# Optimization experiments

Measured on AMD Instinct MI355X. Metric: run time of the kernel, lower is better.

The kernel has to match this reference:

```python
import jax, jax.numpy as jnp
import numpy as np
from jax import lax

N_SAMPLES = 2 ** 15          # 32768
N_FRAMES = 128
N_HARMONICS = 8
FILT_SIZE = 64
N_EVENTS = 8
N_SCALE = 128                # len(MusicalScale()) assumed = 128 (MIDI notes)
NYQ = 11025.0                # SR22050 nyquist
MIN_F0 = 40.0 / NYQ
MAX_F0 = 3000.0 / NYQ
F0_SPAN = MAX_F0 - MIN_F0
MIN_RES = 0.9
RES_SPAN = 1.0 - MIN_RES
PI = float(np.pi)

# packed layout slices (order of param_sizes dict)
SL_F0 = slice(0, 128)
SL_FINE = slice(128, 256)
SL_AMP = slice(256, 384)
SL_HAMP = slice(384, 392)
SL_HDEC = slice(392, 400)
SL_FENV = slice(400, 464)


def lin_interp(x, out_size):
    """F.interpolate(mode='linear', align_corners=False) along last axis."""
    n = x.shape[-1]
    pos = (jnp.arange(out_size, dtype=x.dtype) + 0.5) * (n / out_size) - 0.5
    pos = jnp.clip(pos, 0.0, n - 1)
    lo = jnp.floor(pos).astype(jnp.int32)
    hi = jnp.minimum(lo + 1, n - 1)
    w = pos - lo.astype(x.dtype)
    return x[..., lo] * (1.0 - w) + x[..., hi] * w


def setup_inputs() -> dict:
    key = jax.random.key(0)
    k1, k2 = jax.random.split(key)
    B = 32 * N_EVENTS  # 256 event rows
    packed = jax.random.normal(k1, (B, 464), dtype=jnp.float32)
    # musical scale: MIDI-note center frequencies normalized by nyquist
    midi = np.arange(N_SCALE)
    freqs = 440.0 * 2.0 ** ((midi - 69) / 12.0) / NYQ
    frequencies = jnp.asarray(freqs, dtype=jnp.float32)
    noise = jax.random.uniform(k2, (B, 1, N_SAMPLES), dtype=jnp.float32)  # mapped to (-1,1) in reference
    return {"packed": packed, "frequencies": frequencies, "noise": noise}


def reference(packed, frequencies, noise):
    B = packed.shape[0]
    p = jax.nn.sigmoid(packed)  # Model applies activation(p) before SynthParams

    # f0: softmax over discrete scale bins, weighted sum of normalized freqs
    f0w = jax.nn.softmax(p[:, SL_F0], axis=-1)             # [B, 128]
    f0 = (f0w @ frequencies)[:, None, None]                # [B,1,1]
    f0 = jnp.broadcast_to(f0, (B, 1, N_FRAMES))            # repeat over frames
    f0 = f0 * NYQ
    f0 = MIN_F0 + f0 * F0_SPAN                             # [B,1,128]
    # NOTE: source computes `f0 + f0 + f0_fine` and discards it -> f0_fine unused

    harmonic_factors = jnp.arange(1, N_HARMONICS + 1, dtype=p.dtype)
    osc = f0 * harmonic_factors[None, :, None]             # [B,8,128]
    radians = osc / NYQ * PI
    radians = lin_interp(radians, N_SAMPLES)               # [B,8,32768]
    osc_bank = jnp.sin(jnp.cumsum(radians, axis=-1))

    harm_decay = MIN_RES + p[:, SL_HDEC] * RES_SPAN        # [B,8]
    harm_amp = p[:, SL_HAMP]                               # [B,8]
    amp = p[:, SL_AMP][:, None, :] * 2.0 - 1.0             # [B,1,128]
    amp_full = lin_interp(amp, N_SAMPLES)                  # [B,1,32768]

    noise_filter = p[:, SL_FENV][:, None, :]               # [B,1,64]
    noise_filter = lin_interp(noise_filter, N_SAMPLES // 2)
    noise_filter = jnp.pad(noise_filter, ((0, 0), (0, 0), (0, 1)))  # [B,1,16385]

    noise_u = noise * 2.0 - 1.0                            # uniform(-1,1)
    noise_spec = jnp.fft.rfft(noise_u, axis=-1, norm='ortho')
    filt = jnp.fft.irfft(noise_spec * noise_filter, n=N_SAMPLES, axis=-1, norm='ortho')
    filt = filt * jnp.clip(amp_full, 0.0, 1.0)             # [B,1,32768]

    # leaky-accumulator recurrence over frames
    def step(cur, a_i):  # cur [B,8], a_i [B]
        cur = jnp.clip(cur + a_i[:, None] * harm_amp, 0.0, 1.0)
        out = cur
        cur = cur * harm_decay
        return cur, out

    amp_t = amp[:, 0, :].T                                 # [128, B]
    _, outs = lax.scan(step, jnp.zeros((B, N_HARMONICS), dtype=p.dtype), amp_t)
    x = jnp.transpose(outs, (1, 2, 0))                     # [B,8,128]
    x = jnp.where(x >= PI, 0.0, x)
    x = lin_interp(x, N_SAMPLES)                           # [B,8,32768]
    x = x * osc_bank
    x = filt + x
    x = x.reshape(-1, N_EVENTS, N_HARMONICS, N_SAMPLES)
    x = jnp.sum(x, axis=(1, 2))[:, None, :]                # [batch,1,32768]
    return x
```

## Files before the change

### kernel.cpp

```cpp
#include <hip/hip_runtime.h>
#include <math.h>

#ifndef M_PI
#define M_PI 3.14159265358979323846
#endif

#define NSAMP 32768
#define MHALF 16384
#define TWO_PI_F 6.2831853071795864f

__device__ __forceinline__ double dsig(double x) { return 1.0 / (1.0 + exp(-x)); }

__global__ __launch_bounds__(128) void prep_kernel(
    const float* __restrict__ packed, const float* __restrict__ freqs,
    unsigned long long* __restrict__ step, float* __restrict__ env,
    float* __restrict__ amp, float* __restrict__ fenv)
{
    int b = blockIdx.x;
    int t = threadIdx.x;
    const float* pk = packed + b * 464;
    __shared__ double sh_num[128];
    __shared__ double sh_den[128];
    __shared__ double amp_d[128];

    double e_t = exp(dsig((double)pk[t]));
    sh_den[t] = e_t;
    sh_num[t] = e_t * (double)freqs[t];

    double av = dsig((double)pk[256 + t]) * 2.0 - 1.0;
    amp_d[t] = av;
    amp[b * 128 + t] = (float)av;

    if (t < 64) fenv[b * 64 + t] = (float)dsig((double)pk[400 + t]);
    __syncthreads();

    for (int off = 64; off > 0; off >>= 1) {
        if (t < off) { sh_den[t] += sh_den[t + off]; sh_num[t] += sh_num[t + off]; }
        __syncthreads();
    }

    if (t < 8) {
        const double NYQ = 11025.0;
        const double MIN_F0 = 40.0 / NYQ;
        const double MAX_F0 = 3000.0 / NYQ;
        const double F0_SPAN = MAX_F0 - MIN_F0;
        double f0 = sh_num[0] / sh_den[0];
        double F = f0 * NYQ;
        double G = MIN_F0 + F * F0_SPAN;
        double oscf = G * (double)(t + 1);
        double r = oscf / NYQ * M_PI;
        double rv = r / (2.0 * M_PI);
        rv -= floor(rv);
        step[b * 8 + t] = (unsigned long long)(rv * 18446744073709551616.0);

        double ha = dsig((double)pk[384 + t]);
        double hd = 0.9 + dsig((double)pk[392 + t]) * (1.0 - 0.9);
        double cur = 0.0;
        float* eo = env + (size_t)(b * 8 + t) * 128;
        for (int fr = 0; fr < 128; fr++) {
            cur = cur + amp_d[fr] * ha;
            cur = fmin(fmax(cur, 0.0), 1.0);
            eo[fr] = (float)cur;
            cur *= hd;
        }
    }
}

__device__ __forceinline__ float2 cmulc(float2 a, float2 b) {
    return make_float2(a.x * b.x - a.y * b.y, a.x * b.y + a.y * b.x);
}
__device__ __forceinline__ float2 twid(float2 a, float ang) {
    float sn, cs; __sincosf(ang, &sn, &cs);
    return make_float2(a.x * cs - a.y * sn, a.x * sn + a.y * cs);
}

template<int INV>
__device__ __forceinline__ void fft4(float2& x0, float2& x1, float2& x2, float2& x3) {
    float2 s02 = make_float2(x0.x + x2.x, x0.y + x2.y);
    float2 d02 = make_float2(x0.x - x2.x, x0.y - x2.y);
    float2 s13 = make_float2(x1.x + x3.x, x1.y + x3.y);
    float2 d13 = make_float2(x1.x - x3.x, x1.y - x3.y);
    float2 j13 = INV ? make_float2(-d13.y, d13.x) : make_float2(d13.y, -d13.x);
    x0 = make_float2(s02.x + s13.x, s02.y + s13.y);
    x2 = make_float2(s02.x - s13.x, s02.y - s13.y);
    x1 = make_float2(d02.x + j13.x, d02.y + j13.y);
    x3 = make_float2(d02.x - j13.x, d02.y - j13.y);
}

#define V16(v, c) v[((((c) & 3) << 2) | ((c) >> 2))]

template<int INV>
__device__ __forceinline__ void fft16(float2 v[16]) {
    const float s = INV ? 1.0f : -1.0f;
#pragma unroll
    for (int b = 0; b < 4; b++) fft4<INV>(v[b], v[4 + b], v[8 + b], v[12 + b]);
    v[5]  = cmulc(v[5],  make_float2(0.9238795325f,  s * 0.3826834324f));
    v[9]  = cmulc(v[9],  make_float2(0.7071067812f,  s * 0.7071067812f));
    v[13] = cmulc(v[13], make_float2(0.3826834324f,  s * 0.9238795325f));
    v[6]  = cmulc(v[6],  make_float2(0.7071067812f,  s * 0.7071067812f));
    v[10] = cmulc(v[10], make_float2(0.0f,           s * 1.0f));
    v[14] = cmulc(v[14], make_float2(-0.7071067812f, s * 0.7071067812f));
    v[7]  = cmulc(v[7],  make_float2(0.3826834324f,  s * 0.9238795325f));
    v[11] = cmulc(v[11], make_float2(-0.7071067812f, s * 0.7071067812f));
    v[15] = cmulc(v[15], make_float2(-0.9238795325f, s * -0.3826834324f));
#pragma unroll
    for (int p = 0; p < 4; p++) fft4<INV>(v[4 * p], v[4 * p + 1], v[4 * p + 2], v[4 * p + 3]);
}

__device__ __forceinline__ int physA(int A) { return A + (A >> 6); }

__device__ __forceinline__ float hinterp64(const float* f, int j) {
    float pos = ((float)j + 0.5f) * (1.0f / 256.0f) - 0.5f;
    pos = fminf(fmaxf(pos, 0.0f), 63.0f);
    int lo = (int)pos;
    int hi = min(lo + 1, 63);
    float w = pos - (float)lo;
    return f[lo] * (1.0f - w) + f[hi] * w;
}

template<int INV>
__device__ __forceinline__ void passes234(float2* z, int tid) {
    const float sgn = INV ? 1.0f : -1.0f;
    const int c0 = tid >> 8;
    {
        const int bp = tid & 255;
        float2 v[16];
        const int base = c0 * 4096 + bp;
#pragma unroll
        for (int a = 0; a < 16; a++) v[a] = z[base + 256 * a];
        __syncthreads();
        fft16<INV>(v);
        const float w0 = sgn * (TWO_PI_F / 4096.f) * (float)bp;
        z[(c0 * 16 + 0) * 257 + bp] = V16(v, 0);
#pragma unroll
        for (int c1 = 1; c1 < 16; c1++)
            z[(c0 * 16 + c1) * 257 + bp] = twid(V16(v, c1), w0 * (float)c1);
        __syncthreads();
    }
    {
        const int c1 = (tid >> 4) & 15, b2 = tid & 15;
        float2 v[16];
        const int base = (c0 * 16 + c1) * 257 + b2;
#pragma unroll
        for (int a = 0; a < 16; a++) v[a] = z[base + 16 * a];
        __syncthreads();
        fft16<INV>(v);
        const float w0 = sgn * (TWO_PI_F / 256.f) * (float)b2;
        z[((c0 * 16 + c1) * 16 + 0) * 17 + b2] = V16(v, 0);
#pragma unroll
        for (int c2 = 1; c2 < 16; c2++)
            z[((c0 * 16 + c1) * 16 + c2) * 17 + b2] = twid(V16(v, c2), w0 * (float)c2);
        __syncthreads();
    }
    {
        const int c1 = (tid >> 4) & 15, c2 = tid & 15;
        float2 v[16];
        const int base = ((c0 * 16 + c1) * 16 + c2) * 17;
#pragma unroll
        for (int b = 0; b < 16; b++) v[b] = z[base + b];
        __syncthreads();
        fft16<INV>(v);
        const int A0 = 64 * c2 + 4 * c1 + c0;
#pragma unroll
        for (int c3 = 0; c3 < 16; c3++) {
            int A = 1024 * c3 + A0;
            z[physA(A)] = V16(v, c3);
        }
        __syncthreads();
    }
}

__global__ __launch_bounds__(1024) void fft_kernel(
    const float* __restrict__ noise, const float* __restrict__ amp,
    const float* __restrict__ fenv, float* __restrict__ filt)
{
    __shared__ float2 z[17408];
    __shared__ float fenv_s[64];
    __shared__ float amp_s[128];
    const int bb = blockIdx.x;
    const int tid = threadIdx.x;

    if (tid < 64) fenv_s[tid] = fenv[bb * 64 + tid];
    if (tid < 128) amp_s[tid] = amp[bb * 128 + tid];

    const float2* nz = (const float2*)(noise + (size_t)bb * NSAMP);

    {
        float2 v[16];
#pragma unroll
        for (int m = 0; m < 4; m++)
#pragma unroll
            for (int a = 0; a < 4; a++) {
                float2 t = nz[a * 4096 + m * 1024 + tid];
                v[m * 4 + a] = make_float2(t.x * 2.f - 1.f, t.y * 2.f - 1.f);
            }
#pragma unroll
        for (int m = 0; m < 4; m++) {
            fft4<0>(v[m * 4 + 0], v[m * 4 + 1], v[m * 4 + 2], v[m * 4 + 3]);
            float w0 = -(TWO_PI_F / 16384.f) * (float)(m * 1024 + tid);
#pragma unroll
            for (int c0 = 1; c0 < 4; c0++) v[m * 4 + c0] = twid(v[m * 4 + c0], w0 * (float)c0);
#pragma unroll
            for (int c0 = 0; c0 < 4; c0++) z[c0 * 4096 + m * 1024 + tid] = v[m * 4 + c0];
        }
    }
    __syncthreads();
    passes234<0>(z, tid);

    const float invM = 1.0f / (float)MHALF;
    for (int k = tid; k <= 8192; k += 1024) {
        if (k == 0) {
            float2 Z0 = z[physA(0)];
            float Y0 = (Z0.x + Z0.y) * hinterp64(fenv_s, 0);
            float vv = Y0 * 0.5f * invM;
            z[physA(0)] = make_float2(vv, vv);
        } else if (k == 8192) {
            float s = hinterp64(fenv_s, 8192) * invM;
            float2 Zk = z[physA(8192)];
            z[physA(8192)] = make_float2(Zk.x * s, Zk.y * s);
        } else {
            int ik = physA(k), imk = physA(16384 - k);
            float2 Zk = z[ik], Zm = z[imk];
            float Ex = 0.5f * (Zk.x + Zm.x);
            float Ey = 0.5f * (Zk.y - Zm.y);
            float Ox = 0.5f * (Zk.y + Zm.y);
            float Oy = -0.5f * (Zk.x - Zm.x);
            float ang = (float)M_PI * (float)k * (1.0f / 16384.0f);
            float sn, cs;
            __sincosf(ang, &sn, &cs);
            float Xkx = Ex + cs * Ox + sn * Oy;
            float Xky = Ey + cs * Oy - sn * Ox;
            float Xmx = Ex - cs * Ox - sn * Oy;
            float Xmy = -Ey + cs * Oy - sn * Ox;
            float Hk = hinterp64(fenv_s, k);
            float Hm = hinterp64(fenv_s, 16384 - k);
            float Ykx = Xkx * Hk, Yky = Xky * Hk;
            float Ymx = Xmx * Hm, Ymy = Xmy * Hm;
            float Er = 0.5f * (Ykx + Ymx);
            float Ei = 0.5f * (Yky - Ymy);
            float Pr = 0.5f * (Ykx - Ymx);
            float Pi = 0.5f * (Yky + Ymy);
            float Oyx = Pr * cs - Pi * sn;
            float Oyy = Pr * sn + Pi * cs;
            z[ik]  = make_float2((Er - Oyy) * invM, (Ei + Oyx) * invM);
            z[imk] = make_float2((Er + Oyy) * invM, (-Ei + Oyx) * invM);
        }
    }
    __syncthreads();

    {
        float2 v[16];
#pragma unroll
        for (int m = 0; m < 4; m++)
#pragma unroll
            for (int a = 0; a < 4; a++) {
                int A = a * 4096 + m * 1024 + tid;
                v[m * 4 + a] = z[physA(A)];
            }
        __syncthreads();
#pragma unroll
        for (int m = 0; m < 4; m++) {
            fft4<1>(v[m * 4 + 0], v[m * 4 + 1], v[m * 4 + 2], v[m * 4 + 3]);
            float w0 = (TWO_PI_F / 16384.f) * (float)(m * 1024 + tid);
#pragma unroll
            for (int c0 = 1; c0 < 4; c0++) v[m * 4 + c0] = twid(v[m * 4 + c0], w0 * (float)c0);
#pragma unroll
            for (int c0 = 0; c0 < 4; c0++) z[c0 * 4096 + m * 1024 + tid] = v[m * 4 + c0];
        }
    }
    __syncthreads();
    passes234<1>(z, tid);

    float2* fo = (float2*)(filt + (size_t)bb * NSAMP);
    for (int m = tid; m < MHALF; m += 1024) {
        float2 y = z[physA(m)];
        int s0 = 2 * m;
        float p0 = ((float)s0 + 0.5f) * (1.0f / 256.0f) - 0.5f;
        float p1 = p0 + (1.0f / 256.0f);
        p0 = fminf(fmaxf(p0, 0.0f), 127.0f);
        p1 = fminf(fmaxf(p1, 0.0f), 127.0f);
        int l0 = (int)p0, l1 = (int)p1;
        int h0 = min(l0 + 1, 127), h1 = min(l1 + 1, 127);
        float w0 = p0 - (float)l0, w1 = p1 - (float)l1;
        float a0 = amp_s[l0] * (1.0f - w0) + amp_s[h0] * w0;
        float a1 = amp_s[l1] * (1.0f - w1) + amp_s[h1] * w1;
        a0 = fminf(fmaxf(a0, 0.0f), 1.0f);
        a1 = fminf(fmaxf(a1, 0.0f), 1.0f);
        fo[m] = make_float2(y.x * a0, y.y * a1);
    }
}

__global__ __launch_bounds__(256) void synth_kernel(
    const unsigned long long* __restrict__ step, const float* __restrict__ env,
    const float* __restrict__ filt, float* __restrict__ out)
{
    const int chunk = blockIdx.x;
    const int g = blockIdx.y;
    const int tid = threadIdx.x;
    __shared__ float env_s[64 * 128];
    __shared__ unsigned long long step_s[64];

    const float* eg = env + (size_t)g * 64 * 128;
    for (int i = tid; i < 64 * 128; i += 256) env_s[i] = eg[i];
    if (tid < 64) step_s[tid] = step[g * 64 + tid];
    __syncthreads();

    const int s0 = chunk * 1024 + tid * 4;

    float4 aF = make_float4(0.f, 0.f, 0.f, 0.f);
#pragma unroll
    for (int e = 0; e < 8; e++) {
        const float4 f = *(const float4*)(filt + ((size_t)(g * 8 + e)) * NSAMP + s0);
        aF.x += f.x; aF.y += f.y; aF.z += f.z; aF.w += f.w;
    }

    float c0v[4], c1v[4], c2v[4];
    int lo0;
    {
        float pos0 = ((float)s0 + 0.5f) * (1.0f / 256.0f) - 0.5f;
        pos0 = fminf(fmaxf(pos0, 0.0f), 127.0f);
        lo0 = (int)pos0;
        int lo3 = lo0;
#pragma unroll
        for (int k = 0; k < 4; k++) {
            float pos = ((float)(s0 + k) + 0.5f) * (1.0f / 256.0f) - 0.5f;
            pos = fminf(fmaxf(pos, 0.0f), 127.0f);
            int lo = (int)pos;
            float w = pos - (float)lo;
            if (lo == lo0) { c0v[k] = 1.0f - w; c1v[k] = w;        c2v[k] = 0.0f; }
            else           { c0v[k] = 0.0f;     c1v[k] = 1.0f - w; c2v[k] = w;    }
            lo3 = lo;
        }
        (void)lo3;
    }
    const int i1 = min(lo0 + 1, 127);
    int lo3b = lo0;
    {
        float pos = ((float)(s0 + 3) + 0.5f) * (1.0f / 256.0f) - 0.5f;
        pos = fminf(fmaxf(pos, 0.0f), 127.0f);
        lo3b = (int)pos;
    }
    const int i2 = min(lo3b + 1, 127);

    float a0 = 0.f, a1 = 0.f, a2 = 0.f, a3 = 0.f;
    const unsigned long long n0 = (unsigned long long)(unsigned)(s0 + 1);

#pragma unroll 8
    for (int idx = 0; idx < 64; idx++) {
        const unsigned long long st = step_s[idx];
        unsigned long long p = st * n0;
        const float* er = env_s + (idx << 7);
        const float v0 = er[lo0], v1 = er[i1], v2 = er[i2];

        float ev, fr, sn;

        fr = (float)(unsigned)(p >> 32) * 0x1p-32f;
        sn = __builtin_amdgcn_sinf(fr);
        ev = fmaf(v0, c0v[0], fmaf(v1, c1v[0], v2 * c2v[0]));
        a0 = fmaf(ev, sn, a0); p += st;

        fr = (float)(unsigned)(p >> 32) * 0x1p-32f;
        sn = __builtin_amdgcn_sinf(fr);
        ev = fmaf(v0, c0v[1], fmaf(v1, c1v[1], v2 * c2v[1]));
        a1 = fmaf(ev, sn, a1); p += st;

        fr = (float)(unsigned)(p >> 32) * 0x1p-32f;
        sn = __builtin_amdgcn_sinf(fr);
        ev = fmaf(v0, c0v[2], fmaf(v1, c1v[2], v2 * c2v[2]));
        a2 = fmaf(ev, sn, a2); p += st;

        fr = (float)(unsigned)(p >> 32) * 0x1p-32f;
        sn = __builtin_amdgcn_sinf(fr);
        ev = fmaf(v0, c0v[3], fmaf(v1, c1v[3], v2 * c2v[3]));
        a3 = fmaf(ev, sn, a3);
    }

    float4 r;
    r.x = a0 + 8.0f * aF.x;
    r.y = a1 + 8.0f * aF.y;
    r.z = a2 + 8.0f * aF.z;
    r.w = a3 + 8.0f * aF.w;
    *(float4*)(out + (size_t)g * NSAMP + s0) = r;
}

extern "C" void kernel_launch(void* const* d_in, const int* in_sizes, int n_in,
                              void* d_out, int out_size, void* d_ws, size_t ws_size,
                              hipStream_t stream)
{
    (void)in_sizes; (void)n_in; (void)out_size; (void)ws_size;
    const float* packed = (const float*)d_in[0];
    const float* freqs  = (const float*)d_in[1];
    const float* noise  = (const float*)d_in[2];
    float* out = (float*)d_out;
    char* ws = (char*)d_ws;

    unsigned long long* step = (unsigned long long*)(ws);
    float* env  = (float*)(ws + 16384);
    float* amp  = (float*)(ws + 16384 + 1048576);
    float* fenv = (float*)(ws + 16384 + 1048576 + 131072);
    float* filt = (float*)(ws + 16384 + 1048576 + 131072 + 65536);

    hipLaunchKernelGGL(prep_kernel, dim3(256), dim3(128), 0, stream,
                       packed, freqs, step, env, amp, fenv);
    hipLaunchKernelGGL(fft_kernel, dim3(256), dim3(1024), 0, stream,
                       noise, amp, fenv, filt);
    hipLaunchKernelGGL(synth_kernel, dim3(32, 32), dim3(256), 0, stream,
                       step, env, filt, out);
}
```

Baseline: 138.6 us.

## Restructure FFT as 16x1024 planes with wave-local passes and XOR-swizzled LDS

Replaces the 4x16x16x16 shared-memory FFT schedule with a first radix-16 pass across the block, followed by 1024-point sub-FFTs that each 64-thread wavefront performs on its own plane, so the inner passes need no block-wide barriers. The padded layout is replaced by an XOR swizzle to avoid LDS bank conflicts without padding. The inverse FFT's final radix-16 pass now writes directly to global memory with the amplitude envelope applied, skipping a shared-memory round trip. Correctness depends on each plane being touched only by its own wavefront, so later passes rely on intra-wave ordering without __syncthreads, which is fragile.

Result: slower. 155.8 us (+12.4%).

```diff
diff --git a/kernel.cpp b/kernel.cpp
--- a/kernel.cpp
+++ b/kernel.cpp
@@ -107,7 +107,93 @@
     for (int p = 0; p < 4; p++) fft4<INV>(v[4 * p], v[4 * p + 1], v[4 * p + 2], v[4 * p + 3]);
 }
 
-__device__ __forceinline__ int physA(int A) { return A + (A >> 6); }
+__device__ __forceinline__ int zph(int p, int q) {
+    return (p << 10) + (q ^ ((q >> 4) & 15) ^ p);
+}
+__device__ __forceinline__ int zaddr(int k) {
+    int p = k & 15, k2 = k >> 4;
+    int q = 256 * (k2 & 3) + 16 * ((k2 >> 2) & 15) + (k2 >> 6);
+    return zph(p, q);
+}
+
+__device__ __forceinline__ void plane_fwd(float2* Z, int p, int l) {
+    {
+        float2 u[16];
+#pragma unroll
+        for (int j = 0; j < 4; j++)
+#pragma unroll
+            for (int a = 0; a < 4; a++) u[j * 4 + a] = Z[zph(p, 256 * a + 64 * j + l)];
+#pragma unroll
+        for (int j = 0; j < 4; j++) {
+            fft4<0>(u[j * 4 + 0], u[j * 4 + 1], u[j * 4 + 2], u[j * 4 + 3]);
+            float w0 = -(TWO_PI_F / 1024.f) * (float)(64 * j + l);
+#pragma unroll
+            for (int k4 = 1; k4 < 4; k4++) u[j * 4 + k4] = twid(u[j * 4 + k4], w0 * (float)k4);
+#pragma unroll
+            for (int k4 = 0; k4 < 4; k4++) Z[zph(p, 256 * k4 + 64 * j + l)] = u[j * 4 + k4];
+        }
+    }
+    {
+        const int k4 = l >> 4, c = l & 15;
+        float2 v[16];
+#pragma unroll
+        for (int b = 0; b < 16; b++) v[b] = Z[zph(p, 256 * k4 + 16 * b + c)];
+        fft16<0>(v);
+        const float w0 = -(TWO_PI_F / 256.f) * (float)c;
+        Z[zph(p, 256 * k4 + c)] = V16(v, 0);
+#pragma unroll
+        for (int kb = 1; kb < 16; kb++)
+            Z[zph(p, 256 * k4 + 16 * kb + c)] = twid(V16(v, kb), w0 * (float)kb);
+    }
+    {
+        const int base = 256 * (l >> 4) + 16 * (l & 15);
+        float2 v[16];
+#pragma unroll
+        for (int c = 0; c < 16; c++) v[c] = Z[zph(p, base + c)];
+        fft16<0>(v);
+#pragma unroll
+        for (int kc = 0; kc < 16; kc++) Z[zph(p, base + kc)] = V16(v, kc);
+    }
+}
+
+__device__ __forceinline__ void plane_inv(float2* Z, int p, int l) {
+    {
+        const int kb = l & 15;
+        const int base = 256 * (l >> 4) + 16 * kb;
+        float2 v[16];
+#pragma unroll
+        for (int kc = 0; kc < 16; kc++) v[kc] = Z[zph(p, base + kc)];
+        fft16<1>(v);
+        const float w0 = (TWO_PI_F / 256.f) * (float)kb;
+        Z[zph(p, base + 0)] = V16(v, 0);
+#pragma unroll
+        for (int nc = 1; nc < 16; nc++)
+            Z[zph(p, base + nc)] = twid(V16(v, nc), w0 * (float)nc);
+    }
+    {
+        const int k4 = l >> 4, nc = l & 15;
+        float2 v[16];
+#pragma unroll
+        for (int kb = 0; kb < 16; kb++) v[kb] = Z[zph(p, 256 * k4 + 16 * kb + nc)];
+        fft16<1>(v);
+        const float w0 = (TWO_PI_F / 1024.f) * (float)k4;
+#pragma unroll
+        for (int nb = 0; nb < 16; nb++) {
+            float2 val = V16(v, nb);
+            if (k4 != 0) val = twid(val, w0 * (float)(16 * nb + nc));
+            Z[zph(p, 256 * k4 + 16 * nb + nc)] = val;
+        }
+    }
+#pragma unroll
+    for (int j = 0; j < 4; j++) {
+        float2 u[4];
+#pragma unroll
+        for (int k4 = 0; k4 < 4; k4++) u[k4] = Z[zph(p, 256 * k4 + 64 * j + l)];
+        fft4<1>(u[0], u[1], u[2], u[3]);
+#pragma unroll
+        for (int na = 0; na < 4; na++) Z[zph(p, 256 * na + 64 * j + l)] = u[na];
+    }
+}
 
 __device__ __forceinline__ float hinterp64(const float* f, int j) {
     float pos = ((float)j + 0.5f) * (1.0f / 256.0f) - 0.5f;
@@ -118,67 +204,16 @@
     return f[lo] * (1.0f - w) + f[hi] * w;
 }
 
-template<int INV>
-__device__ __forceinline__ void passes234(float2* z, int tid) {
-    const float sgn = INV ? 1.0f : -1.0f;
-    const int c0 = tid >> 8;
-    {
-        const int bp = tid & 255;
-        float2 v[16];
-        const int base = c0 * 4096 + bp;
-#pragma unroll
-        for (int a = 0; a < 16; a++) v[a] = z[base + 256 * a];
-        __syncthreads();
-        fft16<INV>(v);
-        const float w0 = sgn * (TWO_PI_F / 4096.f) * (float)bp;
-        z[(c0 * 16 + 0) * 257 + bp] = V16(v, 0);
-#pragma unroll
-        for (int c1 = 1; c1 < 16; c1++)
-            z[(c0 * 16 + c1) * 257 + bp] = twid(V16(v, c1), w0 * (float)c1);
-        __syncthreads();
-    }
-    {
-        const int c1 = (tid >> 4) & 15, b2 = tid & 15;
-        float2 v[16];
-        const int base = (c0 * 16 + c1) * 257 + b2;
-#pragma unroll
-        for (int a = 0; a < 16; a++) v[a] = z[base + 16 * a];
-        __syncthreads();
-        fft16<INV>(v);
-        const float w0 = sgn * (TWO_PI_F / 256.f) * (float)b2;
-        z[((c0 * 16 + c1) * 16 + 0) * 17 + b2] = V16(v, 0);
-#pragma unroll
-        for (int c2 = 1; c2 < 16; c2++)
-            z[((c0 * 16 + c1) * 16 + c2) * 17 + b2] = twid(V16(v, c2), w0 * (float)c2);
-        __syncthreads();
-    }
-    {
-        const int c1 = (tid >> 4) & 15, c2 = tid & 15;
-        float2 v[16];
-        const int base = ((c0 * 16 + c1) * 16 + c2) * 17;
-#pragma unroll
-        for (int b = 0; b < 16; b++) v[b] = z[base + b];
-        __syncthreads();
-        fft16<INV>(v);
-        const int A0 = 64 * c2 + 4 * c1 + c0;
-#pragma unroll
-        for (int c3 = 0; c3 < 16; c3++) {
-            int A = 1024 * c3 + A0;
-            z[physA(A)] = V16(v, c3);
-        }
-        __syncthreads();
-    }
-}
-
 __global__ __launch_bounds__(1024) void fft_kernel(
     const float* __restrict__ noise, const float* __restrict__ amp,
     const float* __restrict__ fenv, float* __restrict__ filt)
 {
-    __shared__ float2 z[17408];
+    __shared__ float2 Z[16384];
     __shared__ float fenv_s[64];
     __shared__ float amp_s[128];
     const int bb = blockIdx.x;
     const int tid = threadIdx.x;
+    const int w = tid >> 6, l = tid & 63;
 
     if (tid < 64) fenv_s[tid] = fenv[bb * 64 + tid];
     if (tid < 128) amp_s[tid] = amp[bb * 128 + tid];
@@ -188,39 +223,38 @@
     {
         float2 v[16];
 #pragma unroll
-        for (int m = 0; m < 4; m++)
-#pragma unroll
-            for (int a = 0; a < 4; a++) {
-                float2 t = nz[a * 4096 + m * 1024 + tid];
-                v[m * 4 + a] = make_float2(t.x * 2.f - 1.f, t.y * 2.f - 1.f);
-            }
-#pragma unroll
-        for (int m = 0; m < 4; m++) {
-            fft4<0>(v[m * 4 + 0], v[m * 4 + 1], v[m * 4 + 2], v[m * 4 + 3]);
-            float w0 = -(TWO_PI_F / 16384.f) * (float)(m * 1024 + tid);
-#pragma unroll
-            for (int c0 = 1; c0 < 4; c0++) v[m * 4 + c0] = twid(v[m * 4 + c0], w0 * (float)c0);
-#pragma unroll
-            for (int c0 = 0; c0 < 4; c0++) z[c0 * 4096 + m * 1024 + tid] = v[m * 4 + c0];
-        }
-    }
-    __syncthreads();
-    passes234<0>(z, tid);
+        for (int a = 0; a < 16; a++) {
+            float2 t = nz[a * 1024 + tid];
+            v[a] = make_float2(t.x * 2.f - 1.f, t.y * 2.f - 1.f);
+        }
+        fft16<0>(v);
+        const float w0 = -(TWO_PI_F / 16384.f) * (float)tid;
+        Z[zph(0, tid)] = V16(v, 0);
+#pragma unroll
+        for (int k1 = 1; k1 < 16; k1++)
+            Z[zph(k1, tid)] = twid(V16(v, k1), w0 * (float)k1);
+    }
+    __syncthreads();
+
+    plane_fwd(Z, w, l);
+    __syncthreads();
 
     const float invM = 1.0f / (float)MHALF;
     for (int k = tid; k <= 8192; k += 1024) {
         if (k == 0) {
-            float2 Z0 = z[physA(0)];
+            int i0 = zaddr(0);
+            float2 Z0 = Z[i0];
             float Y0 = (Z0.x + Z0.y) * hinterp64(fenv_s, 0);
             float vv = Y0 * 0.5f * invM;
-            z[physA(0)] = make_float2(vv, vv);
+            Z[i0] = make_float2(vv, vv);
         } else if (k == 8192) {
+            int i8 = zaddr(8192);
             float s = hinterp64(fenv_s, 8192) * invM;
-            float2 Zk = z[physA(8192)];
-            z[physA(8192)] = make_float2(Zk.x * s, Zk.y * s);
+            float2 Zk = Z[i8];
+            Z[i8] = make_float2(Zk.x * s, Zk.y * s);
         } else {
-            int ik = physA(k), imk = physA(16384 - k);
-            float2 Zk = z[ik], Zm = z[imk];
+            int ik = zaddr(k), imk = zaddr(16384 - k);
+            float2 Zk = Z[ik], Zm = Z[imk];
             float Ex = 0.5f * (Zk.x + Zm.x);
             float Ey = 0.5f * (Zk.y - Zm.y);
             float Ox = 0.5f * (Zk.y + Zm.y);
@@ -242,51 +276,43 @@
             float Pi = 0.5f * (Yky + Ymy);
             float Oyx = Pr * cs - Pi * sn;
             float Oyy = Pr * sn + Pi * cs;
-            z[ik]  = make_float2((Er - Oyy) * invM, (Ei + Oyx) * invM);
-            z[imk] = make_float2((Er + Oyy) * invM, (-Ei + Oyx) * invM);
-        }
-    }
-    __syncthreads();
-
-    {
-        float2 v[16];
-#pragma unroll
-        for (int m = 0; m < 4; m++)
-#pragma unroll
-            for (int a = 0; a < 4; a++) {
-                int A = a * 4096 + m * 1024 + tid;
-                v[m * 4 + a] = z[physA(A)];
-            }
-        __syncthreads();
-#pragma unroll
-        for (int m = 0; m < 4; m++) {
-            fft4<1>(v[m * 4 + 0], v[m * 4 + 1], v[m * 4 + 2], v[m * 4 + 3]);
-            float w0 = (TWO_PI_F / 16384.f) * (float)(m * 1024 + tid);
-#pragma unroll
-            for (int c0 = 1; c0 < 4; c0++) v[m * 4 + c0] = twid(v[m * 4 + c0], w0 * (float)c0);
-#pragma unroll
-            for (int c0 = 0; c0 < 4; c0++) z[c0 * 4096 + m * 1024 + tid] = v[m * 4 + c0];
-        }
-    }
-    __syncthreads();
-    passes234<1>(z, tid);
-
-    float2* fo = (float2*)(filt + (size_t)bb * NSAMP);
-    for (int m = tid; m < MHALF; m += 1024) {
-        float2 y = z[physA(m)];
-        int s0 = 2 * m;
-        float p0 = ((float)s0 + 0.5f) * (1.0f / 256.0f) - 0.5f;
-        float p1 = p0 + (1.0f / 256.0f);
-        p0 = fminf(fmaxf(p0, 0.0f), 127.0f);
-        p1 = fminf(fmaxf(p1, 0.0f), 127.0f);
-        int l0 = (int)p0, l1 = (int)p1;
-        int h0 = min(l0 + 1, 127), h1 = min(l1 + 1, 127);
-        float w0 = p0 - (float)l0, w1 = p1 - (float)l1;
-        float a0 = amp_s[l0] * (1.0f - w0) + amp_s[h0] * w0;
-        float a1 = amp_s[l1] * (1.0f - w1) + amp_s[h1] * w1;
-        a0 = fminf(fmaxf(a0, 0.0f), 1.0f);
-        a1 = fminf(fmaxf(a1, 0.0f), 1.0f);
-        fo[m] = make_float2(y.x * a0, y.y * a1);
+            Z[ik]  = make_float2((Er - Oyy) * invM, (Ei + Oyx) * invM);
+            Z[imk] = make_float2((Er + Oyy) * invM, (-Ei + Oyx) * invM);
+        }
+    }
+    __syncthreads();
+
+    plane_inv(Z, w, l);
+    __syncthreads();
+
+    {
+        float2 v[16];
+#pragma unroll
+        for (int k1 = 0; k1 < 16; k1++) v[k1] = Z[zph(k1, tid)];
+        const float w0 = (TWO_PI_F / 16384.f) * (float)tid;
+#pragma unroll
+        for (int k1 = 1; k1 < 16; k1++) v[k1] = twid(v[k1], w0 * (float)k1);
+        fft16<1>(v);
+
+        float2* fo = (float2*)(filt + (size_t)bb * NSAMP);
+#pragma unroll
+        for (int m = 0; m < 16; m++) {
+            float2 y = V16(v, m);
+            int A = m * 1024 + tid;
+            int s0 = 2 * A;
+            float p0 = ((float)s0 + 0.5f) * (1.0f / 256.0f) - 0.5f;
+            float p1 = p0 + (1.0f / 256.0f);
+            p0 = fminf(fmaxf(p0, 0.0f), 127.0f);
+            p1 = fminf(fmaxf(p1, 0.0f), 127.0f);
+            int l0 = (int)p0, l1 = (int)p1;
+            int h0 = min(l0 + 1, 127), h1 = min(l1 + 1, 127);
+            float w0a = p0 - (float)l0, w1a = p1 - (float)l1;
+            float a0 = amp_s[l0] * (1.0f - w0a) + amp_s[h0] * w0a;
+            float a1 = amp_s[l1] * (1.0f - w1a) + amp_s[h1] * w1a;
+            a0 = fminf(fmaxf(a0, 0.0f), 1.0f);
+            a1 = fminf(fmaxf(a1, 0.0f), 1.0f);
+            fo[A] = make_float2(y.x * a0, y.y * a1);
+        }
     }
 }
 
@@ -320,7 +346,6 @@
         float pos0 = ((float)s0 + 0.5f) * (1.0f / 256.0f) - 0.5f;
         pos0 = fminf(fmaxf(pos0, 0.0f), 127.0f);
         lo0 = (int)pos0;
-        int lo3 = lo0;
 #pragma unroll
         for (int k = 0; k < 4; k++) {
             float pos = ((float)(s0 + k) + 0.5f) * (1.0f / 256.0f) - 0.5f;
@@ -329,9 +354,7 @@
             float w = pos - (float)lo;
             if (lo == lo0) { c0v[k] = 1.0f - w; c1v[k] = w;        c2v[k] = 0.0f; }
             else           { c0v[k] = 0.0f;     c1v[k] = 1.0f - w; c2v[k] = w;    }
-            lo3 = lo;
-        }
-        (void)lo3;
+        }
     }
     const int i1 = min(lo0 + 1, 127);
     int lo3b = lo0;
```
